# Kernel optimization log

Measured on AMD Instinct MI355X. Metric: run time of the kernel, lower is better.

The kernel has to match this reference:

```python
import jax, jax.numpy as jnp
import numpy as np

H, C = 8, 16          # heads, per-head dim; hidden = H*C = 128
NEG_SLOPE = 0.2       # GATConv default
EPS = 1e-5            # GraphNorm eps


def setup_inputs() -> dict:
    key = jax.random.key(0)
    ks = iter(jax.random.split(key, 64))
    Np, Na, D, E = 100000, 50000, 128, 500000
    s = 1.0 / np.sqrt(D)

    def w(shape, scale=1.0):
        return jax.random.normal(next(ks), shape, jnp.float32) * scale

    inp = {
        'x_paper': w((Np, D)),
        'x_author': w((Na, D)),
        'edge_writes': jnp.stack([
            jax.random.randint(next(ks), (E,), 0, Na),
            jax.random.randint(next(ks), (E,), 0, Np)]).astype(jnp.int32),
        'edge_cites': jnp.stack([
            jax.random.randint(next(ks), (E,), 0, Np),
            jax.random.randint(next(ks), (E,), 0, Np)]).astype(jnp.int32),
        'W_lin_paper': w((D, 128), s), 'b_lin_paper': jnp.zeros((128,), jnp.float32),
        'W_lin_author': w((D, 128), s), 'b_lin_author': jnp.zeros((128,), jnp.float32),
        'Wsrc_writes': w((128, 128), s), 'Wdst_writes': w((128, 128), s),
        'atts_writes': w((H, C), 0.1), 'attd_writes': w((H, C), 0.1),
        'bias_writes': jnp.zeros((128,), jnp.float32),
        'Wsrc_cites': w((128, 128), s), 'Wdst_cites': w((128, 128), s),
        'atts_cites': w((H, C), 0.1), 'attd_cites': w((H, C), 0.1),
        'bias_cites': jnp.zeros((128,), jnp.float32),
        'gnw_paper': jnp.ones((128,), jnp.float32), 'gnb_paper': jnp.zeros((128,), jnp.float32),
        'gnm_paper': jnp.ones((128,), jnp.float32),
        'gnw_author': jnp.ones((128,), jnp.float32), 'gnb_author': jnp.zeros((128,), jnp.float32),
        'gnm_author': jnp.ones((128,), jnp.float32),
        'W2_paper': w((128, 128), s), 'b2_paper': jnp.zeros((128,), jnp.float32),
        'W2_author': w((128, 128), s), 'b2_author': jnp.zeros((128,), jnp.float32),
    }
    return inp


def _gat(src_emb, dst_emb, ei, Wsrc, Wdst, att_s, att_d, bias, n_dst):
    # PyG GATConv, bipartite input, concat=True, add_self_loops=True (eval / no dropout)
    n_self = min(src_emb.shape[0], n_dst)
    loops = jnp.arange(n_self, dtype=ei.dtype)
    src = jnp.concatenate([ei[0], loops])
    dst = jnp.concatenate([ei[1], loops])
    xs = (src_emb @ Wsrc).reshape(-1, H, C)          # [Ns,H,C]
    xd = (dst_emb @ Wdst).reshape(-1, H, C)          # [Nd,H,C]
    a_s = (xs * att_s).sum(-1)                       # [Ns,H]
    a_d = (xd * att_d).sum(-1)                       # [Nd,H]
    e = jax.nn.leaky_relu(a_s[src] + a_d[dst], NEG_SLOPE)   # [E,H]
    m = jax.ops.segment_max(e, dst, num_segments=n_dst)
    m = jnp.where(jnp.isfinite(m), m, 0.0)           # guard empty segments
    p = jnp.exp(e - m[dst])
    denom = jax.ops.segment_sum(p, dst, num_segments=n_dst)
    alpha = p / (denom[dst] + 1e-16)                 # segment softmax over dst
    msg = xs[src] * alpha[:, :, None]                # [E,H,C]
    out = jax.ops.segment_sum(msg, dst, num_segments=n_dst)  # [Nd,H,C]
    return out.reshape(n_dst, H * C) + bias


def _gnorm(x, w, b, ms):
    mu = x.mean(0)
    o = x - ms * mu
    var = (o * o).mean(0)
    return w * o * jax.lax.rsqrt(var + EPS) + b


def reference(x_paper, x_author, edge_writes, edge_cites,
              W_lin_paper, b_lin_paper, W_lin_author, b_lin_author,
              Wsrc_writes, Wdst_writes, atts_writes, attd_writes, bias_writes,
              Wsrc_cites, Wdst_cites, atts_cites, attd_cites, bias_cites,
              gnw_paper, gnb_paper, gnm_paper, gnw_author, gnb_author, gnm_author,
              W2_paper, b2_paper, W2_author, b2_author):
    emb_p = jax.nn.relu(x_paper @ W_lin_paper + b_lin_paper)
    emb_a = jax.nn.relu(x_author @ W_lin_author + b_lin_author)
    Np = emb_p.shape[0]
    out_p = _gat(emb_a, emb_p, edge_writes, Wsrc_writes, Wdst_writes,
                 atts_writes, attd_writes, bias_writes, Np)
    out_p = out_p + _gat(emb_p, emb_p, edge_cites, Wsrc_cites, Wdst_cites,
                         atts_cites, attd_cites, bias_cites, Np)
    out_a = jnp.zeros((emb_a.shape[0], H * C), x_author.dtype)  # no edge type targets author
    out_p = _gnorm(out_p, gnw_paper, gnb_paper, gnm_paper) @ W2_paper + b2_paper
    out_a = _gnorm(out_a, gnw_author, gnb_author, gnm_author) @ W2_author + b2_author
    return (out_p, out_a)
```

## Files before the change

### kernel.cpp

```cpp
#include <hip/hip_runtime.h>
#include <cstdint>
#include <cstddef>

#define H 8
#define DHID 128
#define BM 64
#define LDST 136
#define NEG_SLOPE 0.2f
#define GN_EPS 1e-5f

#define SCAN_T 256
#define SCAN_I 4

typedef __attribute__((ext_vector_type(8))) short short8;
typedef __attribute__((ext_vector_type(4))) float f32x4;

__device__ __forceinline__ void atomAddF(float* p, float v) {
    __hip_atomic_fetch_add(p, v, __ATOMIC_RELAXED, __HIP_MEMORY_SCOPE_AGENT);
}
__device__ __forceinline__ unsigned short f2bf(float f) {
    uint32_t u = __float_as_uint(f);
    uint32_t r = (u + 0x7FFFu + ((u >> 16) & 1u)) >> 16;
    return (unsigned short)r;
}
__device__ __forceinline__ float bflo(uint32_t v) { return __uint_as_float(v << 16); }
__device__ __forceinline__ float bfhi(uint32_t v) { return __uint_as_float(v & 0xFFFF0000u); }

struct PrepHist {
    const float *Wlp, *Wsc, *Wla, *Wsw, *W2p;
    const float *Wdw, *adw, *asc_, *Wdc, *adc_, *asw_;
    unsigned short *WlinP_p, *WsrcP_c, *WlinP_a, *WsrcP_w, *W2P_p, *VscP_p, *VscP_a;
    const float *bw, *bc, *gnb_a, *W2a, *b2a;
    float *bsum, *row_a, *colsum, *colsumsq;
    unsigned short *xs_w_ph, *xs_c_ph;
    float *as_w_ph, *as_c_ph;
    const int *dst_w, *dst_c;
    int *deg, *rank;
    int Ew, nself_w, Ec, nself_c, Np, HB0;
};

__global__ void prep_hist(PrepHist a) {
    int b = blockIdx.x, t = threadIdx.x;
    if (b >= a.HB0) {
        int i = (b - a.HB0) * 256 + t;
        int tw = a.Ew + a.nself_w;
        if (i < tw) {
            int d = (i < a.Ew) ? a.dst_w[i] : (i - a.Ew);
            a.rank[i] = atomicAdd(&a.deg[d], 1);
        } else {
            int j = i - tw;
            if (j < a.Ec + a.nself_c) {
                int d = (j < a.Ec) ? a.dst_c[j] : (j - a.Ec);
                a.rank[i] = atomicAdd(&a.deg[a.Np + d], 1);
            }
        }
        return;
    }
    if (b == 56) {
        if (t < 128) {
            a.bsum[t] = a.bw[t] + a.bc[t];
            float acc = a.b2a[t];
            for (int k = 0; k < DHID; ++k) acc += a.gnb_a[k] * a.W2a[k * DHID + t];
            a.row_a[t] = acc;
            a.colsum[t] = 0.f;
            a.colsumsq[t] = 0.f;
            a.xs_w_ph[t] = 0;
            a.xs_c_ph[t] = 0;
        } else if (t < 136) a.as_w_ph[t - 128] = -1e30f;
        else if (t < 144) a.as_c_ph[t - 136] = -1e30f;
        return;
    }
    int j = b >> 3;
    int idx = (b & 7) * 256 + t;
    int lane = idx & 63, kk = (idx >> 6) & 3, nt = idx >> 8;
    int col = nt * 16 + (lane & 15);
    int k0 = kk * 32 + ((lane >> 4) << 3);
    if (j < 5) {
        const float* W = j == 0 ? a.Wlp : j == 1 ? a.Wsc : j == 2 ? a.Wla : j == 3 ? a.Wsw : a.W2p;
        unsigned short* out = j == 0 ? a.WlinP_p : j == 1 ? a.WsrcP_c : j == 2 ? a.WlinP_a
                              : j == 3 ? a.WsrcP_w : a.W2P_p;
        for (int i = 0; i < 8; ++i) out[idx * 8 + i] = f2bf(W[(k0 + i) * DHID + col]);
    } else if (j == 5) {
        if (idx >= 2 * 256) return;
        const float *W = nullptr, *A = nullptr;
        int h = col & 7;
        if (col < 24) {
            int which = col >> 3;
            W = which == 0 ? a.Wdw : which == 1 ? a.Wsc : a.Wdc;
            A = which == 0 ? a.adw : which == 1 ? a.asc_ : a.adc_;
        }
        for (int i = 0; i < 8; ++i) {
            float v = 0.f;
            if (W)
                for (int c = 0; c < 16; ++c) v += W[(k0 + i) * DHID + h * 16 + c] * A[h * 16 + c];
            a.VscP_p[idx * 8 + i] = f2bf(v);
        }
    } else {
        if (idx >= 256) return;
        int h = col & 7;
        for (int i = 0; i < 8; ++i) {
            float v = 0.f;
            if (col < 8)
                for (int c = 0; c < 16; ++c)
                    v += a.Wsw[(k0 + i) * DHID + h * 16 + c] * a.asw_[h * 16 + c];
            a.VscP_a[idx * 8 + i] = f2bf(v);
        }
    }
}

__global__ void scan1(const int* __restrict__ in, int n, int* __restrict__ out,
                      int* __restrict__ bsums, int pad, int* __restrict__ totalOut) {
    __shared__ int sh[SCAN_T];
    int t = threadIdx.x;
    long base = (long)blockIdx.x * SCAN_T * SCAN_I;
    int v[SCAN_I];
    int s = 0;
#pragma unroll
    for (int j = 0; j < SCAN_I; ++j) {
        long idx = base + (long)t * SCAN_I + j;
        int x = (idx < n) ? in[idx] : 0;
        if (pad) x = (x + 3) & ~3;
        v[j] = x;
        s += x;
    }
    sh[t] = s;
    __syncthreads();
    for (int off = 1; off < SCAN_T; off <<= 1) {
        int x = (t >= off) ? sh[t - off] : 0;
        __syncthreads();
        sh[t] += x;
        __syncthreads();
    }
    int run = sh[t] - s;
#pragma unroll
    for (int j = 0; j < SCAN_I; ++j) {
        long idx = base + (long)t * SCAN_I + j;
        if (idx < n) out[idx] = run;
        run += v[j];
    }
    if (t == SCAN_T - 1) {
        bsums[blockIdx.x] = sh[SCAN_T - 1];
        if (totalOut) *totalOut = sh[SCAN_T - 1];
    }
}

__global__ void scan3_prefill(const int* __restrict__ off_raw, const int* __restrict__ bs1,
                              int n2, int* __restrict__ off2,
                              int Np, int Na, int maxTot, int* __restrict__ srcu) {
    int i = blockIdx.x * 256 + threadIdx.x;
    if (i < n2) off2[i] = off_raw[i] + bs1[i / (SCAN_T * SCAN_I)];
    int mid = off_raw[Np] + bs1[Np / (SCAN_T * SCAN_I)];
    long stride = (long)gridDim.x * 256;
    for (long k = i; k < maxTot; k += stride) srcu[k] = (k < (long)mid) ? Na : Np;
}

template <int NSC>
__device__ void proj_body(unsigned short* xt, int bid,
                          const float* __restrict__ x, int nrows,
                          const unsigned short* __restrict__ WlinP, const float* __restrict__ blin,
                          const unsigned short* __restrict__ WsrcP,
                          const unsigned short* __restrict__ VscP,
                          unsigned short* __restrict__ xs,
                          float* __restrict__ a0, float* __restrict__ a1, float* __restrict__ a2) {
    int t = threadIdx.x;
    int lane = t & 63, w = t >> 6;
    long row0 = (long)bid * BM;
    for (int it = 0; it < 16; ++it) {
        int idx2 = t + it * 256;
        int r = idx2 >> 6, cp = idx2 & 63;
        long gr = row0 + r;
        float v0 = 0.f, v1 = 0.f;
        if (gr < nrows) { v0 = x[gr * DHID + 2 * cp]; v1 = x[gr * DHID + 2 * cp + 1]; }
        uint32_t pk = (uint32_t)f2bf(v0) | ((uint32_t)f2bf(v1) << 16);
        *reinterpret_cast<uint32_t*>(&xt[r * LDST + 2 * cp]) = pk;
    }
    __syncthreads();
    int arow = w * 16 + (lane & 15);
    int koff = (lane >> 4) << 3;
    short8 af[4];
#pragma unroll
    for (int kk = 0; kk < 4; ++kk)
        af[kk] = *reinterpret_cast<const short8*>(&xt[arow * LDST + kk * 32 + koff]);
    const short8* Bl = reinterpret_cast<const short8*>(WlinP);
    f32x4 acc[8];
#pragma unroll
    for (int nt = 0; nt < 8; ++nt) {
        f32x4 a = {0.f, 0.f, 0.f, 0.f};
#pragma unroll
        for (int kk = 0; kk < 4; ++kk)
            a = __builtin_amdgcn_mfma_f32_16x16x32_bf16(af[kk], Bl[(nt * 4 + kk) * 64 + lane], a, 0, 0, 0);
        acc[nt] = a;
    }
    __syncthreads();
    int orow = w * 16 + ((lane >> 4) << 2);
    int ccol = lane & 15;
#pragma unroll
    for (int nt = 0; nt < 8; ++nt) {
        float b = blin[nt * 16 + ccol];
#pragma unroll
        for (int r = 0; r < 4; ++r) {
            float e = fmaxf(acc[nt][r] + b, 0.f);
            xt[(orow + r) * LDST + nt * 16 + ccol] = f2bf(e);
        }
    }
    __syncthreads();
#pragma unroll
    for (int kk = 0; kk < 4; ++kk)
        af[kk] = *reinterpret_cast<const short8*>(&xt[arow * LDST + kk * 32 + koff]);
    const short8* Bs = reinterpret_cast<const short8*>(WsrcP);
#pragma unroll
    for (int nt = 0; nt < 8; ++nt) {
        f32x4 a = {0.f, 0.f, 0.f, 0.f};
#pragma unroll
        for (int kk = 0; kk < 4; ++kk)
            a = __builtin_amdgcn_mfma_f32_16x16x32_bf16(af[kk], Bs[(nt * 4 + kk) * 64 + lane], a, 0, 0, 0);
        acc[nt] = a;
    }
    const short8* Bv = reinterpret_cast<const short8*>(VscP);
    f32x4 sacc0 = {0.f, 0.f, 0.f, 0.f}, sacc1 = {0.f, 0.f, 0.f, 0.f};
#pragma unroll
    for (int kk = 0; kk < 4; ++kk)
        sacc0 = __builtin_amdgcn_mfma_f32_16x16x32_bf16(af[kk], Bv[kk * 64 + lane], sacc0, 0, 0, 0);
    if (NSC > 1) {
#pragma unroll
        for (int kk = 0; kk < 4; ++kk)
            sacc1 = __builtin_amdgcn_mfma_f32_16x16x32_bf16(af[kk], Bv[(4 + kk) * 64 + lane], sacc1, 0, 0, 0);
    }
#pragma unroll
    for (int nt = 0; nt < 8; ++nt) {
#pragma unroll
        for (int r = 0; r < 4; ++r) {
            long gr = row0 + orow + r;
            if (gr < nrows) xs[gr * DHID + nt * 16 + ccol] = f2bf(acc[nt][r]);
        }
    }
#pragma unroll
    for (int st = 0; st < NSC; ++st) {
        int scol = st * 16 + ccol;
        int h = scol & 7, which = scol >> 3;
        float* ap = which == 0 ? a0 : which == 1 ? a1 : which == 2 ? a2 : nullptr;
        if (ap) {
            f32x4 s = st == 0 ? sacc0 : sacc1;
#pragma unroll
            for (int r = 0; r < 4; ++r) {
                long gr = row0 + orow + r;
                if (gr < nrows) ap[gr * H + h] = s[r];
            }
        }
    }
}

struct MegaArgs {
    const float* x_p; int Np;
    const unsigned short* WlinP_p; const float* blp;
    const unsigned short* WsrcP_c; const unsigned short* VscP_p;
    unsigned short* xs_c; float *a_d_w, *a_s_c, *a_d_c;
    const float* x_a; int Na;
    const unsigned short* WlinP_a; const float* bla;
    const unsigned short* WsrcP_w; const unsigned short* VscP_a;
    unsigned short* xs_w; float* a_s_w;
    const int *src_w, *dst_w, *src_c, *dst_c;
    int Ew, nself_w, Ec, nself_c;
    const int *off2, *rank;
    int* srcu;
    int PB, AB;
};

__global__ __launch_bounds__(256) void mega(MegaArgs a) {
    __shared__ unsigned short xt[BM * LDST];
    int b = blockIdx.x;
    int G = gridDim.x;
    int nP = a.PB + a.AB;
    long fb  = (long)b * nP / G;
    long fb1 = (long)(b + 1) * nP / G;
    if (fb1 > fb) {
        int pb = (int)fb;
        if (pb < a.PB)
            proj_body<2>(xt, pb, a.x_p, a.Np, a.WlinP_p, a.blp, a.WsrcP_c, a.VscP_p,
                         a.xs_c, a.a_d_w, a.a_s_c, a.a_d_c);
        else
            proj_body<1>(xt, pb - a.PB, a.x_a, a.Na, a.WlinP_a, a.bla, a.WsrcP_w, a.VscP_a,
                         a.xs_w, a.a_s_w, nullptr, nullptr);
        return;
    }
    int sb = b - (int)fb;
    int i = sb * 256 + threadIdx.x;
    int tw = a.Ew + a.nself_w;
    int s, di;
    if (i < tw) {
        if (i < a.Ew) { s = a.src_w[i]; di = a.dst_w[i]; } else { s = di = i - a.Ew; }
    } else {
        int j = i - tw;
        if (j >= a.Ec + a.nself_c) return;
        if (j < a.Ec) { s = a.src_c[j]; di = a.Np + a.dst_c[j]; }
        else { s = j - a.Ec; di = a.Np + (j - a.Ec); }
    }
    a.srcu[a.off2[di] + a.rank[i]] = s;
}

__global__ __launch_bounds__(256) void gat_gather(
    const int* __restrict__ off, const int* __restrict__ srcu,
    const float* __restrict__ a_s_w, const float* __restrict__ a_d_w,
    const float* __restrict__ a_s_c, const float* __restrict__ a_d_c,
    const unsigned short* __restrict__ xs_w, const unsigned short* __restrict__ xs_c,
    float* __restrict__ gat, int Np) {
    int l = threadIdx.x & 63;
    int d = blockIdx.x * 4 + (threadIdx.x >> 6);
    if (d >= Np) return;
    int h = l >> 3;
    int iw = off[d], w1 = off[d + 1];
    int ic = off[Np + d], c1 = off[Np + d + 1];
    float adw = a_d_w[(long)d * H + h];
    float adc = a_d_c[(long)d * H + h];
    float denw = 0.f, n0w = 0.f, n1w = 0.f;
    float denc = 0.f, n0c = 0.f, n1c = 0.f;
    while (iw < w1 || ic < c1) {
        bool hw = iw < w1, hc = ic < c1;
        int4 sw, sc;
        if (hw) sw = *reinterpret_cast<const int4*>(srcu + iw);
        if (hc) sc = *reinterpret_cast<const int4*>(srcu + ic);
        float ew[4], ec[4];
        uint32_t vw[4], vc[4];
        if (hw) {
            ew[0] = a_s_w[(long)sw.x * H + h];
            ew[1] = a_s_w[(long)sw.y * H + h];
            ew[2] = a_s_w[(long)sw.z * H + h];
            ew[3] = a_s_w[(long)sw.w * H + h];
            vw[0] = *reinterpret_cast<const uint32_t*>(xs_w + (long)sw.x * DHID + 2 * l);
            vw[1] = *reinterpret_cast<const uint32_t*>(xs_w + (long)sw.y * DHID + 2 * l);
            vw[2] = *reinterpret_cast<const uint32_t*>(xs_w + (long)sw.z * DHID + 2 * l);
            vw[3] = *reinterpret_cast<const uint32_t*>(xs_w + (long)sw.w * DHID + 2 * l);
        }
        if (hc) {
            ec[0] = a_s_c[(long)sc.x * H + h];
            ec[1] = a_s_c[(long)sc.y * H + h];
            ec[2] = a_s_c[(long)sc.z * H + h];
            ec[3] = a_s_c[(long)sc.w * H + h];
            vc[0] = *reinterpret_cast<const uint32_t*>(xs_c + (long)sc.x * DHID + 2 * l);
            vc[1] = *reinterpret_cast<const uint32_t*>(xs_c + (long)sc.y * DHID + 2 * l);
            vc[2] = *reinterpret_cast<const uint32_t*>(xs_c + (long)sc.z * DHID + 2 * l);
            vc[3] = *reinterpret_cast<const uint32_t*>(xs_c + (long)sc.w * DHID + 2 * l);
        }
        if (hw) {
#pragma unroll
            for (int j = 0; j < 4; ++j) {
                float e = ew[j] + adw;
                e = e > 0.f ? e : NEG_SLOPE * e;
                float p = __expf(e);
                denw += p;
                n0w += p * bflo(vw[j]);
                n1w += p * bfhi(vw[j]);
            }
            iw += 4;
        }
        if (hc) {
#pragma unroll
            for (int j = 0; j < 4; ++j) {
                float e = ec[j] + adc;
                e = e > 0.f ? e : NEG_SLOPE * e;
                float p = __expf(e);
                denc += p;
                n0c += p * bflo(vc[j]);
                n1c += p * bfhi(vc[j]);
            }
            ic += 4;
        }
    }
    float rw = 1.f / (denw + 1e-16f);
    float rc = 1.f / (denc + 1e-16f);
    float2 o;
    o.x = n0w * rw + n0c * rc;
    o.y = n1w * rw + n1c * rc;
    *reinterpret_cast<float2*>(&gat[(long)d * DHID + 2 * l]) = o;
}

#define GN_ROWS 128
__global__ void gn_reduce(const float* __restrict__ gat, const float* __restrict__ bsum,
                          float* __restrict__ colsum, float* __restrict__ colsumsq, int Np) {
    int t = threadIdx.x;
    long r0 = (long)blockIdx.x * GN_ROWS;
    long r1 = min(r0 + GN_ROWS, (long)Np);
    float b = bsum[t], s1 = 0.f, s2 = 0.f;
    for (long r = r0; r < r1; ++r) {
        float xv = gat[r * DHID + t] + b;
        s1 += xv;
        s2 += xv * xv;
    }
    atomAddF(colsum + t, s1);
    atomAddF(colsumsq + t, s2);
}

__global__ __launch_bounds__(256) void final_fill(
    const float* __restrict__ gat, const float* __restrict__ bsum,
    const float* __restrict__ colsum, const float* __restrict__ colsumsq,
    const float* __restrict__ gnw, const float* __restrict__ gnb,
    const float* __restrict__ gnm,
    const unsigned short* __restrict__ W2P, const float* __restrict__ b2,
    float* __restrict__ out, int Np, int FB,
    const float* __restrict__ row_a, float4* __restrict__ outa, long n4) {
    __shared__ unsigned short xt[BM * LDST];
    __shared__ float cscale[DHID], cshift[DHID];
    int b = blockIdx.x;
    int t = threadIdx.x;
    if (b >= FB) {
        long i = (long)(b - FB) * 256 + t;
        long stride = (long)(gridDim.x - FB) * 256;
        const float4* r4 = reinterpret_cast<const float4*>(row_a);
        for (; i < n4; i += stride) outa[i] = r4[i & 31];
        return;
    }
    int lane = t & 63, w = t >> 6;
    long row0 = (long)b * BM;
    if (t < DHID) {
        float invN = 1.f / (float)Np;
        float mu = colsum[t] * invN;
        float ms = gnm[t];
        float var = colsumsq[t] * invN - mu * mu * ms * (2.f - ms);
        float sc = gnw[t] * rsqrtf(var + GN_EPS);
        cscale[t] = sc;
        cshift[t] = (bsum[t] - ms * mu) * sc + gnb[t];
    }
    __syncthreads();
    for (int it = 0; it < 16; ++it) {
        int idx2 = t + it * 256;
        int r = idx2 >> 6, cp = idx2 & 63;
        long gr = row0 + r;
        float v0 = 0.f, v1 = 0.f;
        if (gr < Np) {
            v0 = gat[gr * DHID + 2 * cp] * cscale[2 * cp] + cshift[2 * cp];
            v1 = gat[gr * DHID + 2 * cp + 1] * cscale[2 * cp + 1] + cshift[2 * cp + 1];
        }
        uint32_t pk = (uint32_t)f2bf(v0) | ((uint32_t)f2bf(v1) << 16);
        *reinterpret_cast<uint32_t*>(&xt[r * LDST + 2 * cp]) = pk;
    }
    __syncthreads();
    int arow = w * 16 + (lane & 15);
    int koff = (lane >> 4) << 3;
    short8 af[4];
#pragma unroll
    for (int kk = 0; kk < 4; ++kk)
        af[kk] = *reinterpret_cast<const short8*>(&xt[arow * LDST + kk * 32 + koff]);
    const short8* Bw = reinterpret_cast<const short8*>(W2P);
    int orow = w * 16 + ((lane >> 4) << 2);
    int ccol = lane & 15;
#pragma unroll
    for (int nt = 0; nt < 8; ++nt) {
        f32x4 a = {0.f, 0.f, 0.f, 0.f};
#pragma unroll
        for (int kk = 0; kk < 4; ++kk)
            a = __builtin_amdgcn_mfma_f32_16x16x32_bf16(af[kk], Bw[(nt * 4 + kk) * 64 + lane], a, 0, 0, 0);
        float bb = b2[nt * 16 + ccol];
#pragma unroll
        for (int r = 0; r < 4; ++r) {
            long gr = row0 + orow + r;
            if (gr < Np) out[gr * DHID + nt * 16 + ccol] = a[r] + bb;
        }
    }
}

extern "C" void kernel_launch(void* const* d_in, const int* in_sizes, int n_in,
                              void* d_out, int out_size, void* d_ws, size_t ws_size,
                              hipStream_t stream) {
    const float* x_p   = (const float*)d_in[0];
    const float* x_a   = (const float*)d_in[1];
    const int*   e_w   = (const int*)d_in[2];
    const int*   e_c   = (const int*)d_in[3];
    const float* Wlp   = (const float*)d_in[4];
    const float* blp   = (const float*)d_in[5];
    const float* Wla   = (const float*)d_in[6];
    const float* bla   = (const float*)d_in[7];
    const float* Wsw   = (const float*)d_in[8];
    const float* Wdw   = (const float*)d_in[9];
    const float* asw   = (const float*)d_in[10];
    const float* adw   = (const float*)d_in[11];
    const float* bw    = (const float*)d_in[12];
    const float* Wsc   = (const float*)d_in[13];
    const float* Wdc   = (const float*)d_in[14];
    const float* asc   = (const float*)d_in[15];
    const float* adc   = (const float*)d_in[16];
    const float* bc    = (const float*)d_in[17];
    const float* gnw_p = (const float*)d_in[18];
    const float* gnb_p = (const float*)d_in[19];
    const float* gnm_p = (const float*)d_in[20];
    const float* gnb_a = (const float*)d_in[22];
    const float* W2p   = (const float*)d_in[24];
    const float* b2p   = (const float*)d_in[25];
    const float* W2a   = (const float*)d_in[26];
    const float* b2a   = (const float*)d_in[27];

    int Np = in_sizes[0] / DHID;
    int Na = in_sizes[1] / DHID;
    int Ew = in_sizes[2] / 2;
    int Ec = in_sizes[3] / 2;
    int nself_w = Na < Np ? Na : Np;
    int nself_c = Np;
    int tot_all = (Ew + nself_w) + (Ec + nself_c);
    int maxTot = tot_all + 6 * Np + 8;

    float* ws = (float*)d_ws;
    float* gat   = ws;
    float* a_d_w = gat + (size_t)Np * DHID;
    float* a_d_c = a_d_w + (size_t)Np * H;
    float* a_s_w = a_d_c + (size_t)Np * H;
    float* a_s_c = a_s_w + (size_t)(Na + 1) * H;
    float* bsum  = a_s_c + (size_t)(Np + 1) * H;
    float* row_a = bsum + DHID;
    float* colsum   = row_a + DHID;
    float* colsumsq = colsum + DHID;
    int*   deg   = (int*)(colsumsq + DHID);
    int* off_raw = deg + 2 * Np;
    int* off2    = off_raw + 2 * Np;
    int* bs1     = off2 + 2 * Np + 1;
    int* bs2     = bs1 + 512;
    uintptr_t up = (uintptr_t)(bs2 + 512);
    up = (up + 15) & ~(uintptr_t)15;
    int* srcu = (int*)up;
    int* rank = srcu + maxTot;
    unsigned short* xs_w = (unsigned short*)(rank + tot_all);
    unsigned short* xs_c = xs_w + (size_t)(Na + 1) * DHID;
    up = (uintptr_t)(xs_c + (size_t)(Np + 1) * DHID);
    up = (up + 15) & ~(uintptr_t)15;
    unsigned short* WlinP_p = (unsigned short*)up;
    unsigned short* WsrcP_c = WlinP_p + 16384;
    unsigned short* WlinP_a = WsrcP_c + 16384;
    unsigned short* WsrcP_w = WlinP_a + 16384;
    unsigned short* W2P_p   = WsrcP_w + 16384;
    unsigned short* VscP_p  = W2P_p + 16384;
    unsigned short* VscP_a  = VscP_p + 4096;

    hipMemsetAsync(deg, 0, 2 * (size_t)Np * sizeof(int), stream);

    int HB = (tot_all + 255) / 256;
    {
        PrepHist pa;
        pa.Wlp = Wlp; pa.Wsc = Wsc; pa.Wla = Wla; pa.Wsw = Wsw; pa.W2p = W2p;
        pa.Wdw = Wdw; pa.adw = adw; pa.asc_ = asc; pa.Wdc = Wdc; pa.adc_ = adc; pa.asw_ = asw;
        pa.WlinP_p = WlinP_p; pa.WsrcP_c = WsrcP_c; pa.WlinP_a = WlinP_a;
        pa.WsrcP_w = WsrcP_w; pa.W2P_p = W2P_p; pa.VscP_p = VscP_p; pa.VscP_a = VscP_a;
        pa.bw = bw; pa.bc = bc; pa.gnb_a = gnb_a; pa.W2a = W2a; pa.b2a = b2a;
        pa.bsum = bsum; pa.row_a = row_a; pa.colsum = colsum; pa.colsumsq = colsumsq;
        pa.xs_w_ph = xs_w + (size_t)Na * DHID;
        pa.xs_c_ph = xs_c + (size_t)Np * DHID;
        pa.as_w_ph = a_s_w + (size_t)Na * H;
        pa.as_c_ph = a_s_c + (size_t)Np * H;
        pa.dst_w = e_w + Ew; pa.dst_c = e_c + Ec;
        pa.deg = deg; pa.rank = rank;
        pa.Ew = Ew; pa.nself_w = nself_w; pa.Ec = Ec; pa.nself_c = nself_c;
        pa.Np = Np; pa.HB0 = 57;
        prep_hist<<<57 + HB, 256, 0, stream>>>(pa);
    }

    int n2 = 2 * Np;
    int nb = (n2 + SCAN_T * SCAN_I - 1) / (SCAN_T * SCAN_I);
    scan1<<<nb, SCAN_T, 0, stream>>>(deg, n2, off_raw, bs1, 1, nullptr);
    scan1<<<1, SCAN_T, 0, stream>>>(bs1, nb, bs1, bs2, 0, off2 + n2);

    scan3_prefill<<<(maxTot + 255) / 256, 256, 0, stream>>>(
        off_raw, bs1, n2, off2, Np, Na, maxTot, srcu);

    {
        MegaArgs ma;
        ma.x_p = x_p; ma.Np = Np; ma.WlinP_p = WlinP_p; ma.blp = blp;
        ma.WsrcP_c = WsrcP_c; ma.VscP_p = VscP_p;
        ma.xs_c = xs_c; ma.a_d_w = a_d_w; ma.a_s_c = a_s_c; ma.a_d_c = a_d_c;
        ma.x_a = x_a; ma.Na = Na; ma.WlinP_a = WlinP_a; ma.bla = bla;
        ma.WsrcP_w = WsrcP_w; ma.VscP_a = VscP_a;
        ma.xs_w = xs_w; ma.a_s_w = a_s_w;
        ma.src_w = e_w; ma.dst_w = e_w + Ew; ma.src_c = e_c; ma.dst_c = e_c + Ec;
        ma.Ew = Ew; ma.nself_w = nself_w; ma.Ec = Ec; ma.nself_c = nself_c;
        ma.off2 = off2; ma.rank = rank; ma.srcu = srcu;
        ma.PB = (Np + BM - 1) / BM;
        ma.AB = (Na + BM - 1) / BM;
        int SB = (tot_all + 255) / 256;
        mega<<<ma.PB + ma.AB + SB, 256, 0, stream>>>(ma);
    }

    gat_gather<<<(Np + 3) / 4, 256, 0, stream>>>(off2, srcu,
                                                 a_s_w, a_d_w, a_s_c, a_d_c,
                                                 xs_w, xs_c, gat, Np);

    gn_reduce<<<(Np + GN_ROWS - 1) / GN_ROWS, 128, 0, stream>>>(gat, bsum, colsum, colsumsq, Np);

    {
        int FB = (Np + BM - 1) / BM;
        long n4 = (long)Na * DHID / 4;
        final_fill<<<FB + 391, 256, 0, stream>>>(
            gat, bsum, colsum, colsumsq, gnw_p, gnb_p, gnm_p, W2P_p, b2p,
            (float*)d_out, Np, FB,
            row_a, (float4*)((float*)d_out + (size_t)Np * DHID), n4);
    }
}
```

Measured before the change: 311.0 us.

## Store GAT output in bf16, fold block-sum scan into prefill, simplify mega dispatch

The intermediate GAT aggregation buffer is now stored as packed bf16 pairs instead of fp32, which halves its write traffic in gat_gather and its read traffic in gn_reduce and final_fill. gn_reduce is restructured to read packed pairs with four row-groups per block over larger row tiles. The single-block second-level scan launch is removed, and each scan3_prefill block recomputes the block-sum prefix in shared memory. The mega kernel now assigns projection blocks first instead of interleaving them with scatter blocks. Rounding to bf16 before the GraphNorm statistics adds precision loss, and the redundant per-block prefix scan adds a little work.

```diff
diff --git a/kernel.cpp b/kernel.cpp
--- a/kernel.cpp
+++ b/kernel.cpp
@@ -22,6 +22,9 @@
     uint32_t u = __float_as_uint(f);
     uint32_t r = (u + 0x7FFFu + ((u >> 16) & 1u)) >> 16;
     return (unsigned short)r;
+}
+__device__ __forceinline__ uint32_t pack2bf(float lo, float hi) {
+    return (uint32_t)f2bf(lo) | ((uint32_t)f2bf(hi) << 16);
 }
 __device__ __forceinline__ float bflo(uint32_t v) { return __uint_as_float(v << 16); }
 __device__ __forceinline__ float bfhi(uint32_t v) { return __uint_as_float(v & 0xFFFF0000u); }
@@ -109,7 +112,7 @@
 }
 
 __global__ void scan1(const int* __restrict__ in, int n, int* __restrict__ out,
-                      int* __restrict__ bsums, int pad, int* __restrict__ totalOut) {
+                      int* __restrict__ bsums) {
     __shared__ int sh[SCAN_T];
     int t = threadIdx.x;
     long base = (long)blockIdx.x * SCAN_T * SCAN_I;
@@ -119,7 +122,7 @@
     for (int j = 0; j < SCAN_I; ++j) {
         long idx = base + (long)t * SCAN_I + j;
         int x = (idx < n) ? in[idx] : 0;
-        if (pad) x = (x + 3) & ~3;
+        x = (x + 3) & ~3;
         v[j] = x;
         s += x;
     }
@@ -138,18 +141,30 @@
         if (idx < n) out[idx] = run;
         run += v[j];
     }
-    if (t == SCAN_T - 1) {
-        bsums[blockIdx.x] = sh[SCAN_T - 1];
-        if (totalOut) *totalOut = sh[SCAN_T - 1];
-    }
+    if (t == SCAN_T - 1) bsums[blockIdx.x] = sh[SCAN_T - 1];
 }
 
 __global__ void scan3_prefill(const int* __restrict__ off_raw, const int* __restrict__ bs1,
-                              int n2, int* __restrict__ off2,
+                              int nb, int n2, int* __restrict__ off2,
                               int Np, int Na, int maxTot, int* __restrict__ srcu) {
-    int i = blockIdx.x * 256 + threadIdx.x;
-    if (i < n2) off2[i] = off_raw[i] + bs1[i / (SCAN_T * SCAN_I)];
-    int mid = off_raw[Np] + bs1[Np / (SCAN_T * SCAN_I)];
+    __shared__ int pf[SCAN_T];
+    int t = threadIdx.x;
+    pf[t] = (t < nb) ? bs1[t] : 0;
+    __syncthreads();
+    for (int off = 1; off < SCAN_T; off <<= 1) {
+        int x = (t >= off) ? pf[t - off] : 0;
+        __syncthreads();
+        pf[t] += x;
+        __syncthreads();
+    }
+    int i = blockIdx.x * 256 + t;
+    if (i < n2) {
+        int g = i >> 10;
+        off2[i] = off_raw[i] + (g ? pf[g - 1] : 0);
+    }
+    if (blockIdx.x == 0 && t == 0) off2[n2] = pf[nb - 1];
+    int gm = Np >> 10;
+    int mid = off_raw[Np] + (gm ? pf[gm - 1] : 0);
     long stride = (long)gridDim.x * 256;
     for (long k = i; k < maxTot; k += stride) srcu[k] = (k < (long)mid) ? Na : Np;
 }
@@ -171,8 +186,7 @@
         long gr = row0 + r;
         float v0 = 0.f, v1 = 0.f;
         if (gr < nrows) { v0 = x[gr * DHID + 2 * cp]; v1 = x[gr * DHID + 2 * cp + 1]; }
-        uint32_t pk = (uint32_t)f2bf(v0) | ((uint32_t)f2bf(v1) << 16);
-        *reinterpret_cast<uint32_t*>(&xt[r * LDST + 2 * cp]) = pk;
+        *reinterpret_cast<uint32_t*>(&xt[r * LDST + 2 * cp]) = pack2bf(v0, v1);
     }
     __syncthreads();
     int arow = w * 16 + (lane & 15);
@@ -269,22 +283,17 @@
 __global__ __launch_bounds__(256) void mega(MegaArgs a) {
     __shared__ unsigned short xt[BM * LDST];
     int b = blockIdx.x;
-    int G = gridDim.x;
-    int nP = a.PB + a.AB;
-    long fb  = (long)b * nP / G;
-    long fb1 = (long)(b + 1) * nP / G;
-    if (fb1 > fb) {
-        int pb = (int)fb;
-        if (pb < a.PB)
-            proj_body<2>(xt, pb, a.x_p, a.Np, a.WlinP_p, a.blp, a.WsrcP_c, a.VscP_p,
-                         a.xs_c, a.a_d_w, a.a_s_c, a.a_d_c);
-        else
-            proj_body<1>(xt, pb - a.PB, a.x_a, a.Na, a.WlinP_a, a.bla, a.WsrcP_w, a.VscP_a,
-                         a.xs_w, a.a_s_w, nullptr, nullptr);
+    if (b < a.PB) {
+        proj_body<2>(xt, b, a.x_p, a.Np, a.WlinP_p, a.blp, a.WsrcP_c, a.VscP_p,
+                     a.xs_c, a.a_d_w, a.a_s_c, a.a_d_c);
         return;
     }
-    int sb = b - (int)fb;
-    int i = sb * 256 + threadIdx.x;
+    if (b < a.PB + a.AB) {
+        proj_body<1>(xt, b - a.PB, a.x_a, a.Na, a.WlinP_a, a.bla, a.WsrcP_w, a.VscP_a,
+                     a.xs_w, a.a_s_w, nullptr, nullptr);
+        return;
+    }
+    int i = (b - a.PB - a.AB) * 256 + threadIdx.x;
     int tw = a.Ew + a.nself_w;
     int s, di;
     if (i < tw) {
@@ -303,7 +312,7 @@
     const float* __restrict__ a_s_w, const float* __restrict__ a_d_w,
     const float* __restrict__ a_s_c, const float* __restrict__ a_d_c,
     const unsigned short* __restrict__ xs_w, const unsigned short* __restrict__ xs_c,
-    float* __restrict__ gat, int Np) {
+    uint32_t* __restrict__ gatb, int Np) {
     int l = threadIdx.x & 63;
     int d = blockIdx.x * 4 + (threadIdx.x >> 6);
     if (d >= Np) return;
@@ -368,30 +377,32 @@
     }
     float rw = 1.f / (denw + 1e-16f);
     float rc = 1.f / (denc + 1e-16f);
-    float2 o;
-    o.x = n0w * rw + n0c * rc;
-    o.y = n1w * rw + n1c * rc;
-    *reinterpret_cast<float2*>(&gat[(long)d * DHID + 2 * l]) = o;
-}
-
-#define GN_ROWS 128
-__global__ void gn_reduce(const float* __restrict__ gat, const float* __restrict__ bsum,
+    gatb[(long)d * 64 + l] = pack2bf(n0w * rw + n0c * rc, n1w * rw + n1c * rc);
+}
+
+#define GN_ROWS 512
+__global__ void gn_reduce(const uint32_t* __restrict__ gatb, const float* __restrict__ bsum,
                           float* __restrict__ colsum, float* __restrict__ colsumsq, int Np) {
     int t = threadIdx.x;
-    long r0 = (long)blockIdx.x * GN_ROWS;
-    long r1 = min(r0 + GN_ROWS, (long)Np);
-    float b = bsum[t], s1 = 0.f, s2 = 0.f;
-    for (long r = r0; r < r1; ++r) {
-        float xv = gat[r * DHID + t] + b;
-        s1 += xv;
-        s2 += xv * xv;
-    }
-    atomAddF(colsum + t, s1);
-    atomAddF(colsumsq + t, s2);
+    int p = t & 63, ro = t >> 6;
+    long r0 = (long)blockIdx.x * GN_ROWS + ro;
+    long r1 = min((long)(blockIdx.x + 1) * GN_ROWS, (long)Np);
+    float b0 = bsum[2 * p], b1 = bsum[2 * p + 1];
+    float s1a = 0.f, s2a = 0.f, s1b = 0.f, s2b = 0.f;
+    for (long r = r0; r < r1; r += 4) {
+        uint32_t u = gatb[r * 64 + p];
+        float x0 = bflo(u) + b0, x1 = bfhi(u) + b1;
+        s1a += x0; s2a += x0 * x0;
+        s1b += x1; s2b += x1 * x1;
+    }
+    atomAddF(colsum + 2 * p, s1a);
+    atomAddF(colsumsq + 2 * p, s2a);
+    atomAddF(colsum + 2 * p + 1, s1b);
+    atomAddF(colsumsq + 2 * p + 1, s2b);
 }
 
 __global__ __launch_bounds__(256) void final_fill(
-    const float* __restrict__ gat, const float* __restrict__ bsum,
+    const uint32_t* __restrict__ gatb, const float* __restrict__ bsum,
     const float* __restrict__ colsum, const float* __restrict__ colsumsq,
     const float* __restrict__ gnw, const float* __restrict__ gnb,
     const float* __restrict__ gnm,
@@ -427,11 +438,11 @@
         long gr = row0 + r;
         float v0 = 0.f, v1 = 0.f;
         if (gr < Np) {
-            v0 = gat[gr * DHID + 2 * cp] * cscale[2 * cp] + cshift[2 * cp];
-            v1 = gat[gr * DHID + 2 * cp + 1] * cscale[2 * cp + 1] + cshift[2 * cp + 1];
-        }
-        uint32_t pk = (uint32_t)f2bf(v0) | ((uint32_t)f2bf(v1) << 16);
-        *reinterpret_cast<uint32_t*>(&xt[r * LDST + 2 * cp]) = pk;
+            uint32_t u = gatb[gr * 64 + cp];
+            v0 = bflo(u) * cscale[2 * cp] + cshift[2 * cp];
+            v1 = bfhi(u) * cscale[2 * cp + 1] + cshift[2 * cp + 1];
+        }
+        *reinterpret_cast<uint32_t*>(&xt[r * LDST + 2 * cp]) = pack2bf(v0, v1);
     }
     __syncthreads();
     int arow = w * 16 + (lane & 15);
@@ -498,8 +509,8 @@
     int maxTot = tot_all + 6 * Np + 8;
 
     float* ws = (float*)d_ws;
-    float* gat   = ws;
-    float* a_d_w = gat + (size_t)Np * DHID;
+    uint32_t* gatb = (uint32_t*)ws;
+    float* a_d_w = (float*)(gatb + (size_t)Np * 64);
     float* a_d_c = a_d_w + (size_t)Np * H;
     float* a_s_w = a_d_c + (size_t)Np * H;
     float* a_s_c = a_s_w + (size_t)(Na + 1) * H;
@@ -511,8 +522,7 @@
     int* off_raw = deg + 2 * Np;
     int* off2    = off_raw + 2 * Np;
     int* bs1     = off2 + 2 * Np + 1;
-    int* bs2     = bs1 + 512;
-    uintptr_t up = (uintptr_t)(bs2 + 512);
+    uintptr_t up = (uintptr_t)(bs1 + 512);
     up = (up + 15) & ~(uintptr_t)15;
     int* srcu = (int*)up;
     int* rank = srcu + maxTot;
@@ -552,11 +562,10 @@
 
     int n2 = 2 * Np;
     int nb = (n2 + SCAN_T * SCAN_I - 1) / (SCAN_T * SCAN_I);
-    scan1<<<nb, SCAN_T, 0, stream>>>(deg, n2, off_raw, bs1, 1, nullptr);
-    scan1<<<1, SCAN_T, 0, stream>>>(bs1, nb, bs1, bs2, 0, off2 + n2);
+    scan1<<<nb, SCAN_T, 0, stream>>>(deg, n2, off_raw, bs1);
 
     scan3_prefill<<<(maxTot + 255) / 256, 256, 0, stream>>>(
-        off_raw, bs1, n2, off2, Np, Na, maxTot, srcu);
+        off_raw, bs1, nb, n2, off2, Np, Na, maxTot, srcu);
 
     {
         MegaArgs ma;
@@ -577,15 +586,15 @@
 
     gat_gather<<<(Np + 3) / 4, 256, 0, stream>>>(off2, srcu,
                                                  a_s_w, a_d_w, a_s_c, a_d_c,
-                                                 xs_w, xs_c, gat, Np);
-
-    gn_reduce<<<(Np + GN_ROWS - 1) / GN_ROWS, 128, 0, stream>>>(gat, bsum, colsum, colsumsq, Np);
+                                                 xs_w, xs_c, gatb, Np);
+
+    gn_reduce<<<(Np + GN_ROWS - 1) / GN_ROWS, 256, 0, stream>>>(gatb, bsum, colsum, colsumsq, Np);
 
     {
         int FB = (Np + BM - 1) / BM;
         long n4 = (long)Na * DHID / 4;
         final_fill<<<FB + 391, 256, 0, stream>>>(
-            gat, bsum, colsum, colsumsq, gnw_p, gnb_p, gnm_p, W2P_p, b2p,
+            gatb, bsum, colsum, colsumsq, gnw_p, gnb_p, gnm_p, W2P_p, b2p,
             (float*)d_out, Np, FB,
             row_a, (float4*)((float*)d_out + (size_t)Np * DHID), n4);
     }
```

New measurement: 305.4 us. About the same (-1.8%).
